# Optimization experiments

Measured on AMD Instinct MI355X. Metric: run time of the kernel, lower is better.

The kernel has to match this reference:

```python
import jax, jax.numpy as jnp
import numpy as np

L, B, D = 2048, 8, 1024
EPS = 1e-5  # torch LayerNorm default


def setup_inputs() -> dict:
    key = jax.random.key(0)
    k1, k2 = jax.random.split(key)
    x = jax.random.normal(k1, (L, B, D), dtype=jnp.float32)
    c = jnp.zeros((B, D), dtype=jnp.float32)
    W_ufr = 0.02 * jax.random.normal(k2, (3 * D, D), dtype=jnp.float32)
    ln_gamma = jnp.ones((D,), dtype=jnp.float32)
    ln_beta = jnp.zeros((D,), dtype=jnp.float32)
    return {"x": x, "c": c, "W_ufr": W_ufr, "ln_gamma": ln_gamma, "ln_beta": ln_beta}


def reference(x, c, W_ufr, ln_gamma, ln_beta):
    # LayerNorm over last dim
    mean = jnp.mean(x, axis=-1, keepdims=True)
    var = jnp.mean(jnp.square(x - mean), axis=-1, keepdims=True)
    x_norm = (x - mean) * jax.lax.rsqrt(var + EPS) * ln_gamma + ln_beta

    # Linear (no bias): [L,B,D] @ [D,3D]
    ufr = jnp.einsum('lbd,ed->lbe', x_norm, W_ufr)
    u, f, r = jnp.split(ufr, 3, axis=-1)
    f_gate = jax.nn.sigmoid(f)
    r_gate = jax.nn.sigmoid(r)

    # Sequential recurrence: c_t = f_t * c_{t-1} + (1 - f_t) * u_t
    def step(c_prev, fu):
        f_t, u_t = fu
        c_t = f_t * c_prev + (1.0 - f_t) * u_t
        return c_t, c_t

    last_c, c_stack = jax.lax.scan(step, c, (f_gate, u))

    hs = r_gate * jnp.tanh(c_stack) + (1.0 - r_gate) * x_norm
    return x + hs, last_c
```

## Files before the change

kernel.cpp:

```cpp
#include <hip/hip_runtime.h>
#include <hip/hip_bf16.h>
#include <stdint.h>

#define L_DIM 2048
#define B_DIM 8
#define D_DIM 1024
#define M_DIM (L_DIM * B_DIM)
#define N_DIM (3 * D_DIM)
#define K_DIM D_DIM
#define CH    (B_DIM * D_DIM)
#define EPSLN 1e-5f
#define NC 128
#define CL (L_DIM / NC)

#define BM 256
#define BN 256
#define BK 64
#define NT (K_DIM / BK)
#define GX (N_DIM / BN)
#define GY (M_DIM / BM)
#define NWG (GX * GY)

typedef __attribute__((ext_vector_type(8))) short short8;
typedef __attribute__((ext_vector_type(4))) float floatx4;

static __device__ __forceinline__ float bf16_lo(unsigned int p) {
    union { unsigned int u; float f; } v; v.u = p << 16; return v.f;
}
static __device__ __forceinline__ float bf16_hi(unsigned int p) {
    union { unsigned int u; float f; } v; v.u = p & 0xffff0000u; return v.f;
}
static __device__ __forceinline__ unsigned short f32_to_bf16(float f) {
    union { float f; unsigned int u; } v;
    v.f = f;
    unsigned int u = v.u;
    u += 0x7fffu + ((u >> 16) & 1u);
    return (unsigned short)(u >> 16);
}
static __device__ __forceinline__ float sigmoidf_fast(float v) {
    return 1.0f / (1.0f + __expf(-v));
}
static __device__ __forceinline__ float tanhf_fast(float c) {
    return 1.0f - 2.0f / (1.0f + __expf(2.0f * c));
}

static __device__ __forceinline__ void async16(const void* g, void* l) {
    __builtin_amdgcn_global_load_lds(
        (const __attribute__((address_space(1))) unsigned int*)g,
        (__attribute__((address_space(3))) unsigned int*)l,
        16, 0, 0);
}

__global__ __launch_bounds__(256) void ln_kernel(const float* __restrict__ x,
                                                 const float* __restrict__ gamma,
                                                 const float* __restrict__ beta,
                                                 unsigned short* __restrict__ xn,
                                                 float* __restrict__ meanOut,
                                                 float* __restrict__ rstdOut) {
    const int wid  = threadIdx.x >> 6;
    const int lane = threadIdx.x & 63;
    const int row  = blockIdx.x * 4 + wid;
    const float* xr = x + (size_t)row * D_DIM;
    float4 v[4];
    float s = 0.0f, s2 = 0.0f;
    #pragma unroll
    for (int j = 0; j < 4; j++) {
        v[j] = *(const float4*)(xr + j * 256 + lane * 4);
        s  += v[j].x + v[j].y + v[j].z + v[j].w;
        s2 += v[j].x * v[j].x + v[j].y * v[j].y + v[j].z * v[j].z + v[j].w * v[j].w;
    }
    #pragma unroll
    for (int o = 32; o > 0; o >>= 1) {
        s  += __shfl_xor(s, o, 64);
        s2 += __shfl_xor(s2, o, 64);
    }
    const float mean = s * (1.0f / D_DIM);
    const float var  = s2 * (1.0f / D_DIM) - mean * mean;
    const float rstd = rsqrtf(var + EPSLN);
    if (lane == 0) { meanOut[row] = mean; rstdOut[row] = rstd; }
    #pragma unroll
    for (int j = 0; j < 4; j++) {
        const int col = j * 256 + lane * 4;
        const float4 g = *(const float4*)(gamma + col);
        const float4 b = *(const float4*)(beta + col);
        unsigned short o0 = f32_to_bf16((v[j].x - mean) * rstd * g.x + b.x);
        unsigned short o1 = f32_to_bf16((v[j].y - mean) * rstd * g.y + b.y);
        unsigned short o2 = f32_to_bf16((v[j].z - mean) * rstd * g.z + b.z);
        unsigned short o3 = f32_to_bf16((v[j].w - mean) * rstd * g.w + b.w);
        uint2 packed;
        packed.x = (unsigned int)o0 | ((unsigned int)o1 << 16);
        packed.y = (unsigned int)o2 | ((unsigned int)o3 << 16);
        *(uint2*)(xn + (size_t)row * D_DIM + col) = packed;
    }
}

__global__ __launch_bounds__(256) void wconv_kernel(const float* __restrict__ W,
                                                    unsigned short* __restrict__ Wb) {
    const size_t i = ((size_t)blockIdx.x * 256 + threadIdx.x) * 4;
    float4 v = *(const float4*)(W + i);
    uint2 packed;
    packed.x = (unsigned int)f32_to_bf16(v.x) | ((unsigned int)f32_to_bf16(v.y) << 16);
    packed.y = (unsigned int)f32_to_bf16(v.z) | ((unsigned int)f32_to_bf16(v.w) << 16);
    *(uint2*)(Wb + i) = packed;
}

__global__ __launch_bounds__(512, 2) void gemm_kernel(const unsigned short* __restrict__ A,
                                                      const unsigned short* __restrict__ W,
                                                      unsigned short* __restrict__ u,
                                                      unsigned short* __restrict__ f,
                                                      unsigned short* __restrict__ r) {
    __shared__ __align__(16) unsigned short ldsA[2 * BM * BK];
    __shared__ __align__(16) unsigned short ldsB[2 * BM * BK];

    const int tid  = threadIdx.x;
    const int wave = tid >> 6;
    const int lane = tid & 63;
    const int quad = lane >> 4;
    const int l16  = lane & 15;
    const int wr   = wave >> 2;
    const int wc   = wave & 3;

    const int orig = blockIdx.y * GX + blockIdx.x;
    const int swz  = (orig & 7) * (NWG / 8) + (orig >> 3);
    const int tx   = swz % GX;
    const int ty   = swz / GX;
    const int m0   = ty * BM;
    const int n0   = tx * BN;

    const int rS = tid >> 3;
    const int kS = ((tid & 7) ^ (rS & 7)) * 8;
    const unsigned short* gA = A + (size_t)(m0 + rS) * K_DIM + kS;
    const unsigned short* gB = W + (size_t)(n0 + rS) * K_DIM + kS;

    const int px     = l16 & 7;
    const int p0_8   = (quad ^ px) * 8;
    const int p1_8   = ((quad + 4) ^ px) * 8;
    const int l16_64 = l16 * 64;
    const int wr4096 = wr * 4096;
    const int wc2048 = wc * 2048;

    floatx4 acc[2][2][4][2] = {};
    short8 aP[2][2], aQ[2][2], b0[2][2], b1[2][2];

#define STAGE_A(BO_, KT_, H_) do { \
    async16(gA + (size_t)((H_) * 128) * K_DIM + (size_t)(KT_) * 64, \
            &ldsA[(BO_) + (H_) * 8192 + (size_t)tid * 8]); \
    async16(gA + (size_t)((H_) * 128 + 64) * K_DIM + (size_t)(KT_) * 64, \
            &ldsA[(BO_) + (H_) * 8192 + 4096 + (size_t)tid * 8]); \
} while (0)

#define STAGE_B(BO_, KT_, H_) do { \
    async16(gB + (size_t)((H_) * 128) * K_DIM + (size_t)(KT_) * 64, \
            &ldsB[(BO_) + (H_) * 8192 + (size_t)tid * 8]); \
    async16(gB + (size_t)((H_) * 128 + 64) * K_DIM + (size_t)(KT_) * 64, \
            &ldsB[(BO_) + (H_) * 8192 + 4096 + (size_t)tid * 8]); \
} while (0)

#define RD_A4(ARR_, BO_, MH_, IH_) do { \
    const unsigned short* pa_ = &ldsA[(BO_) + (MH_) * 8192 + wr4096 + (IH_) * 2048 + l16_64]; \
    ARR_[0][0] = *(const short8*)(pa_ + p0_8); \
    ARR_[0][1] = *(const short8*)(pa_ + p1_8); \
    ARR_[1][0] = *(const short8*)(pa_ + 1024 + p0_8); \
    ARR_[1][1] = *(const short8*)(pa_ + 1024 + p1_8); \
} while (0)

#define RD_B4(ARR_, BO_, NH_) do { \
    const unsigned short* pb_ = &ldsB[(BO_) + (NH_) * 8192 + wc2048 + l16_64]; \
    ARR_[0][0] = *(const short8*)(pb_ + p0_8); \
    ARR_[0][1] = *(const short8*)(pb_ + p1_8); \
    ARR_[1][0] = *(const short8*)(pb_ + 1024 + p0_8); \
    ARR_[1][1] = *(const short8*)(pb_ + 1024 + p1_8); \
} while (0)

#define OCT(ARR_, BRR_, MH_, NH_, IH_) do { \
    __builtin_amdgcn_s_setprio(1); \
    _Pragma("unroll") \
    for (int il_ = 0; il_ < 2; il_++) { \
        _Pragma("unroll") \
        for (int j_ = 0; j_ < 2; j_++) { \
            acc[MH_][NH_][(IH_)*2 + il_][j_] = __builtin_amdgcn_mfma_f32_16x16x32_bf16( \
                ARR_[il_][0], BRR_[j_][0], acc[MH_][NH_][(IH_)*2 + il_][j_], 0, 0, 0); \
            acc[MH_][NH_][(IH_)*2 + il_][j_] = __builtin_amdgcn_mfma_f32_16x16x32_bf16( \
                ARR_[il_][1], BRR_[j_][1], acc[MH_][NH_][(IH_)*2 + il_][j_], 0, 0, 0); \
        } \
    } \
    __builtin_amdgcn_s_setprio(0); \
} while (0)

#define TILE_BARRIER do { \
    asm volatile("s_waitcnt vmcnt(0)" ::: "memory"); \
    __builtin_amdgcn_s_barrier(); \
    __builtin_amdgcn_sched_barrier(0); \
} while (0)

    STAGE_A(0, 0, 0); STAGE_B(0, 0, 0);
    STAGE_A(0, 0, 1); STAGE_B(0, 0, 1);
    TILE_BARRIER;
    RD_A4(aP, 0, 0, 0);
    RD_B4(b0, 0, 0);

    for (int kt = 0; kt < NT - 1; ++kt) {
        const int bufS = (kt & 1) << 14;
        const int nbS  = bufS ^ 16384;
        STAGE_A(nbS, kt + 1, 0); STAGE_B(nbS, kt + 1, 0);
        STAGE_A(nbS, kt + 1, 1); STAGE_B(nbS, kt + 1, 1);
        RD_B4(b1, bufS, 1);
        OCT(aP, b0, 0, 0, 0);
        RD_A4(aQ, bufS, 0, 1);
        OCT(aP, b1, 0, 1, 0);
        RD_A4(aP, bufS, 1, 0);
        OCT(aQ, b0, 0, 0, 1);
        OCT(aQ, b1, 0, 1, 1);
        RD_A4(aQ, bufS, 1, 1);
        TILE_BARRIER;
        OCT(aP, b0, 1, 0, 0);
        OCT(aP, b1, 1, 1, 0);
        RD_A4(aP, nbS, 0, 0);
        OCT(aQ, b0, 1, 0, 1);
        RD_B4(b0, nbS, 0);
        OCT(aQ, b1, 1, 1, 1);
    }

    {
        const int bufS = 16384;
        RD_B4(b1, bufS, 1);
        OCT(aP, b0, 0, 0, 0);
        RD_A4(aQ, bufS, 0, 1);
        OCT(aP, b1, 0, 1, 0);
        RD_A4(aP, bufS, 1, 0);
        OCT(aQ, b0, 0, 0, 1);
        OCT(aQ, b1, 0, 1, 1);
        RD_A4(aQ, bufS, 1, 1);
        OCT(aP, b0, 1, 0, 0);
        OCT(aP, b1, 1, 1, 0);
        OCT(aQ, b0, 1, 0, 1);
        OCT(aQ, b1, 1, 1, 1);
    }

#undef TILE_BARRIER
#undef OCT
#undef RD_B4
#undef RD_A4
#undef STAGE_B
#undef STAGE_A

    const int region = n0 >> 10;
    const int nnb = n0 & 1023;
    unsigned short* dst = (region == 0) ? u : ((region == 1) ? f : r);
    const bool sig = (region != 0);
    #pragma unroll
    for (int mh = 0; mh < 2; mh++) {
        #pragma unroll
        for (int nh = 0; nh < 2; nh++) {
            #pragma unroll
            for (int i = 0; i < 4; i++) {
                #pragma unroll
                for (int j = 0; j < 2; j++) {
                    #pragma unroll
                    for (int t = 0; t < 4; t++) {
                        const int gm = m0 + mh * 128 + wr * 64 + i * 16 + quad * 4 + t;
                        const int nn = nnb + nh * 128 + wc * 32 + j * 16 + l16;
                        float v = acc[mh][nh][i][j][t];
                        if (sig) v = sigmoidf_fast(v);
                        dst[(size_t)gm * D_DIM + nn] = f32_to_bf16(v);
                    }
                }
            }
        }
    }
}

__global__ __launch_bounds__(256) void scan_reduce(const unsigned short* __restrict__ f,
                                                   const unsigned short* __restrict__ u,
                                                   float* __restrict__ Ac,
                                                   float* __restrict__ bc) {
    const int ch4   = (blockIdx.x * 256 + threadIdx.x) * 4;
    const int chunk = blockIdx.y;
    const size_t base = (size_t)chunk * CL * CH + ch4;
    float A0 = 1.0f, A1 = 1.0f, A2 = 1.0f, A3 = 1.0f;
    float b0 = 0.0f, b1 = 0.0f, b2 = 0.0f, b3 = 0.0f;
    #pragma unroll
    for (int i = 0; i < CL; i++) {
        const size_t idx = base + (size_t)i * CH;
        const uint2 fp = *(const uint2*)(f + idx);
        const uint2 up = *(const uint2*)(u + idx);
        const float f0 = bf16_lo(fp.x), f1 = bf16_hi(fp.x);
        const float f2 = bf16_lo(fp.y), f3 = bf16_hi(fp.y);
        const float u0 = bf16_lo(up.x), u1 = bf16_hi(up.x);
        const float u2 = bf16_lo(up.y), u3 = bf16_hi(up.y);
        b0 = f0 * (b0 - u0) + u0;
        b1 = f1 * (b1 - u1) + u1;
        b2 = f2 * (b2 - u2) + u2;
        b3 = f3 * (b3 - u3) + u3;
        A0 *= f0; A1 *= f1; A2 *= f2; A3 *= f3;
    }
    *(float4*)(Ac + chunk * CH + ch4) = make_float4(A0, A1, A2, A3);
    *(float4*)(bc + chunk * CH + ch4) = make_float4(b0, b1, b2, b3);
}

__global__ __launch_bounds__(256) void scan_spine(const float* __restrict__ Ac,
                                                  const float* __restrict__ bc,
                                                  const float* __restrict__ c0,
                                                  float* __restrict__ cst) {
    const int ch = blockIdx.x * 256 + threadIdx.x;
    float c = c0[ch];
    #pragma unroll 16
    for (int j = 0; j < NC; j++) {
        cst[j * CH + ch] = c;
        c = Ac[j * CH + ch] * c + bc[j * CH + ch];
    }
}

__global__ __launch_bounds__(256) void scan_apply(const unsigned short* __restrict__ f,
                                                  const unsigned short* __restrict__ u,
                                                  const unsigned short* __restrict__ r,
                                                  const float* __restrict__ x,
                                                  const float* __restrict__ meanIn,
                                                  const float* __restrict__ rstdIn,
                                                  const float* __restrict__ gamma,
                                                  const float* __restrict__ beta,
                                                  const float* __restrict__ cst,
                                                  float* __restrict__ out,
                                                  float* __restrict__ lastc) {
    const int ch4   = (blockIdx.x * 256 + threadIdx.x) * 4;
    const int chunk = blockIdx.y;
    const int bidx  = ch4 >> 10;
    const int d     = ch4 & 1023;
    const float4 g  = *(const float4*)(gamma + d);
    const float4 be = *(const float4*)(beta + d);
    const size_t base = (size_t)chunk * CL * CH + ch4;
    float4 cc = *(const float4*)(cst + chunk * CH + ch4);
    float c0v = cc.x, c1v = cc.y, c2v = cc.z, c3v = cc.w;
    #pragma unroll 4
    for (int i = 0; i < CL; i++) {
        const int rowLB = (chunk * CL + i) * B_DIM + bidx;
        const float mu = meanIn[rowLB];
        const float rs = rstdIn[rowLB];
        const size_t idx = base + (size_t)i * CH;
        const uint2 fp = *(const uint2*)(f + idx);
        const uint2 up = *(const uint2*)(u + idx);
        const uint2 rp = *(const uint2*)(r + idx);
        const float4 xv = *(const float4*)(x + idx);
        const float f0 = bf16_lo(fp.x), f1 = bf16_hi(fp.x);
        const float f2 = bf16_lo(fp.y), f3 = bf16_hi(fp.y);
        const float u0 = bf16_lo(up.x), u1 = bf16_hi(up.x);
        const float u2 = bf16_lo(up.y), u3 = bf16_hi(up.y);
        c0v = f0 * (c0v - u0) + u0;
        c1v = f1 * (c1v - u1) + u1;
        c2v = f2 * (c2v - u2) + u2;
        c3v = f3 * (c3v - u3) + u3;
        const float r0 = bf16_lo(rp.x), r1 = bf16_hi(rp.x);
        const float r2 = bf16_lo(rp.y), r3 = bf16_hi(rp.y);
        const float n0 = (xv.x - mu) * rs * g.x + be.x;
        const float n1 = (xv.y - mu) * rs * g.y + be.y;
        const float n2 = (xv.z - mu) * rs * g.z + be.z;
        const float n3 = (xv.w - mu) * rs * g.w + be.w;
        float4 o;
        o.x = xv.x + r0 * tanhf_fast(c0v) + (1.0f - r0) * n0;
        o.y = xv.y + r1 * tanhf_fast(c1v) + (1.0f - r1) * n1;
        o.z = xv.z + r2 * tanhf_fast(c2v) + (1.0f - r2) * n2;
        o.w = xv.w + r3 * tanhf_fast(c3v) + (1.0f - r3) * n3;
        *(float4*)(out + idx) = o;
    }
    if (chunk == NC - 1) *(float4*)(lastc + ch4) = make_float4(c0v, c1v, c2v, c3v);
}

extern "C" void kernel_launch(void* const* d_in, const int* in_sizes, int n_in,
                              void* d_out, int out_size, void* d_ws, size_t ws_size,
                              hipStream_t stream) {
    const float* x     = (const float*)d_in[0];
    const float* c0    = (const float*)d_in[1];
    const float* W     = (const float*)d_in[2];
    const float* gamma = (const float*)d_in[3];
    const float* beta  = (const float*)d_in[4];

    float* out   = (float*)d_out;
    float* lastc = out + (size_t)M_DIM * D_DIM;

    char* ws = (char*)d_ws;
    unsigned short* xn = (unsigned short*)ws;  ws += (size_t)M_DIM * K_DIM * 2;
    unsigned short* Wb = (unsigned short*)ws;  ws += (size_t)N_DIM * K_DIM * 2;
    unsigned short* u  = (unsigned short*)ws;  ws += (size_t)M_DIM * D_DIM * 2;
    unsigned short* f  = (unsigned short*)ws;  ws += (size_t)M_DIM * D_DIM * 2;
    unsigned short* r  = (unsigned short*)ws;  ws += (size_t)M_DIM * D_DIM * 2;
    float* meanBuf = (float*)ws;               ws += (size_t)M_DIM * 4;
    float* rstdBuf = (float*)ws;               ws += (size_t)M_DIM * 4;
    float* Ac  = (float*)ws;                   ws += (size_t)NC * CH * 4;
    float* bc  = (float*)ws;                   ws += (size_t)NC * CH * 4;
    float* cst = (float*)ws;                   ws += (size_t)NC * CH * 4;

    ln_kernel<<<M_DIM / 4, 256, 0, stream>>>(x, gamma, beta, xn, meanBuf, rstdBuf);
    wconv_kernel<<<(N_DIM * K_DIM) / 1024, 256, 0, stream>>>(W, Wb);
    gemm_kernel<<<dim3(GX, GY), 512, 0, stream>>>(xn, Wb, u, f, r);
    scan_reduce<<<dim3(CH / 1024, NC), 256, 0, stream>>>(f, u, Ac, bc);
    scan_spine<<<CH / 256, 256, 0, stream>>>(Ac, bc, c0, cst);
    scan_apply<<<dim3(CH / 1024, NC), 256, 0, stream>>>(f, u, r, x, meanBuf, rstdBuf,
                                                        gamma, beta, cst, out, lastc);
}
```

Measured before the change: 292.1 us.

## Restructure GEMM main loop into 8-phase barrier-synchronized ping-pong schedule

```diff
diff --git a/kernel.cpp b/kernel.cpp
--- a/kernel.cpp
+++ b/kernel.cpp
@@ -109,8 +109,8 @@
                                                       unsigned short* __restrict__ u,
                                                       unsigned short* __restrict__ f,
                                                       unsigned short* __restrict__ r) {
-    __shared__ __align__(16) unsigned short ldsA[2 * BM * BK];
-    __shared__ __align__(16) unsigned short ldsB[2 * BM * BK];
+    __shared__ __align__(16) unsigned short ldsA[2][BM * BK];
+    __shared__ __align__(16) unsigned short ldsB[2][BM * BK];
 
     const int tid  = threadIdx.x;
     const int wave = tid >> 6;
@@ -140,107 +140,123 @@
     const int wc2048 = wc * 2048;
 
     floatx4 acc[2][2][4][2] = {};
-    short8 aP[2][2], aQ[2][2], b0[2][2], b1[2][2];
-
-#define STAGE_A(BO_, KT_, H_) do { \
+    short8 a[4][2];
+    short8 b[2][2][2];
+
+#define STAGE_A(BUF_, KT_, H_) do { \
     async16(gA + (size_t)((H_) * 128) * K_DIM + (size_t)(KT_) * 64, \
-            &ldsA[(BO_) + (H_) * 8192 + (size_t)tid * 8]); \
+            &ldsA[BUF_][(H_) * 8192 + (size_t)tid * 8]); \
     async16(gA + (size_t)((H_) * 128 + 64) * K_DIM + (size_t)(KT_) * 64, \
-            &ldsA[(BO_) + (H_) * 8192 + 4096 + (size_t)tid * 8]); \
-} while (0)
-
-#define STAGE_B(BO_, KT_, H_) do { \
+            &ldsA[BUF_][(H_) * 8192 + 4096 + (size_t)tid * 8]); \
+} while (0)
+
+#define STAGE_B(BUF_, KT_, H_) do { \
     async16(gB + (size_t)((H_) * 128) * K_DIM + (size_t)(KT_) * 64, \
-            &ldsB[(BO_) + (H_) * 8192 + (size_t)tid * 8]); \
+            &ldsB[BUF_][(H_) * 8192 + (size_t)tid * 8]); \
     async16(gB + (size_t)((H_) * 128 + 64) * K_DIM + (size_t)(KT_) * 64, \
-            &ldsB[(BO_) + (H_) * 8192 + 4096 + (size_t)tid * 8]); \
-} while (0)
-
-#define RD_A4(ARR_, BO_, MH_, IH_) do { \
-    const unsigned short* pa_ = &ldsA[(BO_) + (MH_) * 8192 + wr4096 + (IH_) * 2048 + l16_64]; \
-    ARR_[0][0] = *(const short8*)(pa_ + p0_8); \
-    ARR_[0][1] = *(const short8*)(pa_ + p1_8); \
-    ARR_[1][0] = *(const short8*)(pa_ + 1024 + p0_8); \
-    ARR_[1][1] = *(const short8*)(pa_ + 1024 + p1_8); \
-} while (0)
-
-#define RD_B4(ARR_, BO_, NH_) do { \
-    const unsigned short* pb_ = &ldsB[(BO_) + (NH_) * 8192 + wc2048 + l16_64]; \
-    ARR_[0][0] = *(const short8*)(pb_ + p0_8); \
-    ARR_[0][1] = *(const short8*)(pb_ + p1_8); \
-    ARR_[1][0] = *(const short8*)(pb_ + 1024 + p0_8); \
-    ARR_[1][1] = *(const short8*)(pb_ + 1024 + p1_8); \
-} while (0)
-
-#define OCT(ARR_, BRR_, MH_, NH_, IH_) do { \
+            &ldsB[BUF_][(H_) * 8192 + 4096 + (size_t)tid * 8]); \
+} while (0)
+
+#define RD_A(BUF_, MH_) do { \
+    const unsigned short* pa_ = &ldsA[BUF_][(MH_) * 8192 + wr4096 + l16_64]; \
+    _Pragma("unroll") \
+    for (int i_ = 0; i_ < 4; i_++) { \
+        a[i_][0] = *(const short8*)(pa_ + i_ * 1024 + p0_8); \
+        a[i_][1] = *(const short8*)(pa_ + i_ * 1024 + p1_8); \
+    } \
+} while (0)
+
+#define RD_B(BUF_, NH_) do { \
+    const unsigned short* pb_ = &ldsB[BUF_][(NH_) * 8192 + wc2048 + l16_64]; \
+    _Pragma("unroll") \
+    for (int j_ = 0; j_ < 2; j_++) { \
+        b[NH_][j_][0] = *(const short8*)(pb_ + j_ * 1024 + p0_8); \
+        b[NH_][j_][1] = *(const short8*)(pb_ + j_ * 1024 + p1_8); \
+    } \
+} while (0)
+
+#define BAR do { \
+    __builtin_amdgcn_s_barrier(); \
+    asm volatile("" ::: "memory"); \
+    __builtin_amdgcn_sched_barrier(0); \
+} while (0)
+#define LGKM0 do { asm volatile("s_waitcnt lgkmcnt(0)" ::: "memory"); \
+                   __builtin_amdgcn_sched_barrier(0); } while (0)
+#define VMW6 asm volatile("s_waitcnt vmcnt(6)" ::: "memory")
+#define VMW0 asm volatile("s_waitcnt vmcnt(0)" ::: "memory")
+
+#define MFMA_Q(MH_, NH_) do { \
     __builtin_amdgcn_s_setprio(1); \
     _Pragma("unroll") \
-    for (int il_ = 0; il_ < 2; il_++) { \
+    for (int i_ = 0; i_ < 4; i_++) { \
         _Pragma("unroll") \
         for (int j_ = 0; j_ < 2; j_++) { \
-            acc[MH_][NH_][(IH_)*2 + il_][j_] = __builtin_amdgcn_mfma_f32_16x16x32_bf16( \
-                ARR_[il_][0], BRR_[j_][0], acc[MH_][NH_][(IH_)*2 + il_][j_], 0, 0, 0); \
-            acc[MH_][NH_][(IH_)*2 + il_][j_] = __builtin_amdgcn_mfma_f32_16x16x32_bf16( \
-                ARR_[il_][1], BRR_[j_][1], acc[MH_][NH_][(IH_)*2 + il_][j_], 0, 0, 0); \
+            acc[MH_][NH_][i_][j_] = __builtin_amdgcn_mfma_f32_16x16x32_bf16( \
+                a[i_][0], b[NH_][j_][0], acc[MH_][NH_][i_][j_], 0, 0, 0); \
+            acc[MH_][NH_][i_][j_] = __builtin_amdgcn_mfma_f32_16x16x32_bf16( \
+                a[i_][1], b[NH_][j_][1], acc[MH_][NH_][i_][j_], 0, 0, 0); \
         } \
     } \
     __builtin_amdgcn_s_setprio(0); \
 } while (0)
 
-#define TILE_BARRIER do { \
-    asm volatile("s_waitcnt vmcnt(0)" ::: "memory"); \
-    __builtin_amdgcn_s_barrier(); \
-    __builtin_amdgcn_sched_barrier(0); \
-} while (0)
-
-    STAGE_A(0, 0, 0); STAGE_B(0, 0, 0);
-    STAGE_A(0, 0, 1); STAGE_B(0, 0, 1);
-    TILE_BARRIER;
-    RD_A4(aP, 0, 0, 0);
-    RD_B4(b0, 0, 0);
-
-    for (int kt = 0; kt < NT - 1; ++kt) {
-        const int bufS = (kt & 1) << 14;
-        const int nbS  = bufS ^ 16384;
-        STAGE_A(nbS, kt + 1, 0); STAGE_B(nbS, kt + 1, 0);
-        STAGE_A(nbS, kt + 1, 1); STAGE_B(nbS, kt + 1, 1);
-        RD_B4(b1, bufS, 1);
-        OCT(aP, b0, 0, 0, 0);
-        RD_A4(aQ, bufS, 0, 1);
-        OCT(aP, b1, 0, 1, 0);
-        RD_A4(aP, bufS, 1, 0);
-        OCT(aQ, b0, 0, 0, 1);
-        OCT(aQ, b1, 0, 1, 1);
-        RD_A4(aQ, bufS, 1, 1);
-        TILE_BARRIER;
-        OCT(aP, b0, 1, 0, 0);
-        OCT(aP, b1, 1, 1, 0);
-        RD_A4(aP, nbS, 0, 0);
-        OCT(aQ, b0, 1, 0, 1);
-        RD_B4(b0, nbS, 0);
-        OCT(aQ, b1, 1, 1, 1);
+    STAGE_A(0, 0, 0); STAGE_B(0, 0, 0); STAGE_B(0, 0, 1); STAGE_A(0, 0, 1);
+    STAGE_A(1, 1, 0); STAGE_B(1, 1, 0); STAGE_B(1, 1, 1);
+    VMW6;
+    BAR;
+
+    for (int i = 0; i < 7; ++i) {
+        const int t = 2 * i;
+        RD_A(0, 0); RD_B(0, 0);
+        STAGE_A(1, t + 1, 1);
+        BAR; LGKM0; MFMA_Q(0, 0); BAR;
+        RD_B(0, 1);
+        STAGE_A(0, t + 2, 0);
+        BAR; LGKM0; MFMA_Q(0, 1); BAR;
+        RD_A(0, 1);
+        STAGE_B(0, t + 2, 0);
+        BAR; LGKM0; MFMA_Q(1, 1); BAR;
+        STAGE_B(0, t + 2, 1);
+        BAR; MFMA_Q(1, 0); VMW6; BAR;
+        RD_A(1, 0); RD_B(1, 0);
+        STAGE_A(0, t + 2, 1);
+        BAR; LGKM0; MFMA_Q(0, 0); BAR;
+        RD_B(1, 1);
+        STAGE_A(1, t + 3, 0);
+        BAR; LGKM0; MFMA_Q(0, 1); BAR;
+        RD_A(1, 1);
+        STAGE_B(1, t + 3, 0);
+        BAR; LGKM0; MFMA_Q(1, 1); BAR;
+        STAGE_B(1, t + 3, 1);
+        BAR; MFMA_Q(1, 0); VMW6; BAR;
     }
 
     {
-        const int bufS = 16384;
-        RD_B4(b1, bufS, 1);
-        OCT(aP, b0, 0, 0, 0);
-        RD_A4(aQ, bufS, 0, 1);
-        OCT(aP, b1, 0, 1, 0);
-        RD_A4(aP, bufS, 1, 0);
-        OCT(aQ, b0, 0, 0, 1);
-        OCT(aQ, b1, 0, 1, 1);
-        RD_A4(aQ, bufS, 1, 1);
-        OCT(aP, b0, 1, 0, 0);
-        OCT(aP, b1, 1, 1, 0);
-        OCT(aQ, b0, 1, 0, 1);
-        OCT(aQ, b1, 1, 1, 1);
-    }
-
-#undef TILE_BARRIER
-#undef OCT
-#undef RD_B4
-#undef RD_A4
+        STAGE_A(1, 15, 1);
+        RD_A(0, 0); RD_B(0, 0);
+        LGKM0; MFMA_Q(0, 0);
+        RD_B(0, 1);
+        LGKM0; MFMA_Q(0, 1);
+        RD_A(0, 1);
+        LGKM0; MFMA_Q(1, 1);
+        MFMA_Q(1, 0);
+        VMW0; BAR;
+        RD_A(1, 0); RD_B(1, 0);
+        LGKM0; MFMA_Q(0, 0);
+        RD_B(1, 1);
+        LGKM0; MFMA_Q(0, 1);
+        RD_A(1, 1);
+        LGKM0; MFMA_Q(1, 1);
+        MFMA_Q(1, 0);
+    }
+
+#undef MFMA_Q
+#undef VMW0
+#undef VMW6
+#undef LGKM0
+#undef BAR
+#undef RD_B
+#undef RD_A
 #undef STAGE_B
 #undef STAGE_A
 
```

Result: no change. 292.1 us (-0.0%).
